# Kernel tuning notes

Measured on AMD Instinct MI355X. Metric: run time of the kernel, lower is better.

Reference implementation:

```python
import jax, jax.numpy as jnp
import numpy as np

N = 1024          # n noisy tokens (seq = 2*N)
DIM = 768
HEADS = 12
HD = DIM // HEADS
BLOCK = 16        # diffusion block size
COND = 128
DFF = 4 * DIM
NEG = -1e30


def rotate_half(x):
    x1, x2 = jnp.split(x, 2, axis=-1)
    return jnp.concatenate((-x2, x1), axis=-1)


def layernorm(x):
    mu = jnp.mean(x, axis=-1, keepdims=True)
    var = jnp.var(x, axis=-1, keepdims=True)
    return (x - mu) * jax.lax.rsqrt(var + 1e-5)


def block_diff_mask(seq, n, block_size):
    idx = jnp.arange(seq)
    q_idx, kv_idx = idx[:, None], idx[None, :]
    fq = q_idx >= n
    fk = kv_idx >= n
    bq = jnp.where(fq, (q_idx - n) // block_size, q_idx // block_size)
    bk = jnp.where(fk, (kv_idx - n) // block_size, kv_idx // block_size)
    block_diagonal = (bq == bk) & (fq == fk)
    offset_block_causal = (bq > bk) & fk & (~fq)
    block_causal = (bq >= bk) & fk & fq
    return block_diagonal | offset_block_causal | block_causal  # [seq, seq] bool


def setup_inputs() -> dict:
    key = jax.random.key(0)
    ks = jax.random.split(key, 12)
    x = jax.random.normal(ks[0], (2, 2 * N, DIM), dtype=jnp.float32)
    c = jax.random.normal(ks[1], (2, COND), dtype=jnp.float32)
    # rotary tables over positions 0..N-1 (each half of the sequence reuses them)
    inv_freq = 1.0 / (10000.0 ** (jnp.arange(0, HD, 2, dtype=jnp.float32) / HD))
    freqs = jnp.arange(N, dtype=jnp.float32)[:, None] * inv_freq[None, :]  # [N, HD/2]
    emb = jnp.concatenate((freqs, freqs), axis=-1)  # [N, HD]
    cos, sin = jnp.cos(emb), jnp.sin(emb)
    s = 0.02
    W_qkv = jax.random.normal(ks[2], (DIM, 3 * DIM), dtype=jnp.float32) * s
    W_out = jax.random.normal(ks[3], (DIM, DIM), dtype=jnp.float32) * s
    ln1_w = jnp.ones((DIM,), dtype=jnp.float32)
    ln2_w = jnp.ones((DIM,), dtype=jnp.float32)
    mlp_w1 = jax.random.normal(ks[4], (DIM, DFF), dtype=jnp.float32) * s
    mlp_b1 = jnp.zeros((DFF,), dtype=jnp.float32)
    mlp_w2 = jax.random.normal(ks[5], (DFF, DIM), dtype=jnp.float32) * s
    mlp_b2 = jnp.zeros((DIM,), dtype=jnp.float32)
    ada_w = jax.random.normal(ks[6], (COND, 6 * DIM), dtype=jnp.float32) * s
    ada_b = jax.random.normal(ks[7], (6 * DIM,), dtype=jnp.float32) * s
    return {"x": x, "cos": cos, "sin": sin, "c": c, "W_qkv": W_qkv, "W_out": W_out,
            "ln1_w": ln1_w, "ln2_w": ln2_w, "mlp_w1": mlp_w1, "mlp_b1": mlp_b1,
            "mlp_w2": mlp_w2, "mlp_b2": mlp_b2, "ada_w": ada_w, "ada_b": ada_b}


def reference(x, cos, sin, c, W_qkv, W_out, ln1_w, ln2_w,
              mlp_w1, mlp_b1, mlp_w2, mlp_b2, ada_w, ada_b):
    b, seq, dim = x.shape
    n = seq // 2
    # adaLN modulation: [b, 1, dim] each (inference: dropout = identity)
    ada = (c @ ada_w + ada_b)[:, None, :]
    shift_msa, scale_msa, gate_msa, shift_mlp, scale_mlp, gate_mlp = jnp.split(ada, 6, axis=2)
    x_skip = x
    h = layernorm(x) * ln1_w
    h = h * (1.0 + scale_msa) + shift_msa  # modulate_fused

    def qkv_rope(seg):
        qkv = (seg @ W_qkv).reshape(b, n, 3, HEADS, HD)
        cs = cos[None, :, None, None, :]
        sn = sin[None, :, None, None, :]
        return qkv * cs + rotate_half(qkv) * sn

    # noisy half and clean (x0) half each get positions 0..n-1
    qkv = jnp.concatenate((qkv_rope(h[:, :n]), qkv_rope(h[:, n:])), axis=1)  # [b,2n,3,H,HD]
    q, k, v = qkv[:, :, 0], qkv[:, :, 1], qkv[:, :, 2]  # [b, 2n, H, HD]
    mask = block_diff_mask(seq, n, BLOCK)  # [2n, 2n]
    scores = jnp.einsum('bqhd,bkhd->bhqk', q, k) / jnp.sqrt(jnp.float32(HD))
    scores = jnp.where(mask[None, None], scores, NEG)
    attn = jax.nn.softmax(scores, axis=-1)
    o = jnp.einsum('bhqk,bkhd->bqhd', attn, v).reshape(b, seq, dim)
    # bias_dropout_add_scale (inference): gate * out + residual
    x1 = gate_msa * (o @ W_out) + x_skip
    h2 = layernorm(x1) * ln2_w
    h2 = h2 * (1.0 + scale_mlp) + shift_mlp
    mlp = jax.nn.gelu(h2 @ mlp_w1 + mlp_b1, approximate=True) @ mlp_w2 + mlp_b2
    return gate_mlp * mlp + x1
```

## Files before the change

### kernel.cpp

```cpp
#include <hip/hip_runtime.h>
#include <hip/hip_bf16.h>
#include <stdint.h>

#define DIM 768
#define SEQ 2048
#define TOKENS 4096
#define HEADS 12
#define DFF 3072
#define COND 128
#define ADA6 4608

typedef __attribute__((ext_vector_type(8))) short bf16x8;
typedef __attribute__((ext_vector_type(4))) float f32x4;

#define MFMA16x32(a, b, c) __builtin_amdgcn_mfma_f32_16x16x32_bf16(a, b, c, 0, 0, 0)
#define GLDS16(g, l)                                                                  \
    __builtin_amdgcn_global_load_lds((const __attribute__((address_space(1))) void*)(g), \
                                     (__attribute__((address_space(3))) void*)(l), 16, 0, 0)

__device__ __forceinline__ ushort f2bf(float f) {
    union { float f; uint32_t u; } v;
    v.f = f;
    uint32_t r = v.u + 0x7FFF + ((v.u >> 16) & 1);
    return (ushort)(r >> 16);
}

__device__ __forceinline__ uint32_t packbf2(float a, float b) {
    union { __hip_bfloat162 h; uint32_t u; } cv;
    cv.h = __float22bfloat162_rn(make_float2(a, b));
    return cv.u;
}

__global__ void ada_kernel(const float* __restrict__ c, const float* __restrict__ ada_w,
                           const float* __restrict__ ada_b, float* __restrict__ ada) {
    int j = blockIdx.x * 256 + threadIdx.x;
    int bb = blockIdx.y;
    if (j < ADA6) {
        float acc = ada_b[j];
        for (int k = 0; k < COND; ++k)
            acc = fmaf(c[bb * COND + k], ada_w[(long)k * ADA6 + j], acc);
        ada[bb * ADA6 + j] = acc;
    }
}

__global__ __launch_bounds__(256) void convT(const float* __restrict__ W,
                                             ushort* __restrict__ Wt, int K, int N) {
    __shared__ float t[64][65];
    int tid = threadIdx.x;
    int n0 = blockIdx.x * 64, k0 = blockIdx.y * 64;
#pragma unroll
    for (int it = 0; it < 4; ++it) {
        int idx = it * 256 + tid;
        int kr = idx >> 4, nc = (idx & 15) * 4;
        float4 v = *(const float4*)&W[(long)(k0 + kr) * N + n0 + nc];
        t[kr][nc] = v.x; t[kr][nc + 1] = v.y; t[kr][nc + 2] = v.z; t[kr][nc + 3] = v.w;
    }
    __syncthreads();
#pragma unroll
    for (int it = 0; it < 4; ++it) {
        int idx = it * 256 + tid;
        int nr = idx >> 4, kc = (idx & 15) * 4;
        ushort4 v;
        v.x = f2bf(t[kc][nr]); v.y = f2bf(t[kc + 1][nr]);
        v.z = f2bf(t[kc + 2][nr]); v.w = f2bf(t[kc + 3][nr]);
        *(ushort4*)&Wt[(long)(n0 + nr) * K + k0 + kc] = v;
    }
}

__global__ __launch_bounds__(256) void ln_mod_kernel(const float* __restrict__ x,
                                                     const float* __restrict__ w,
                                                     const float* __restrict__ ada,
                                                     int shiftOff, int scaleOff,
                                                     ushort* __restrict__ out) {
    int token = blockIdx.x;
    int bb = token >> 11;
    int tid = threadIdx.x;
    const float* xi = x + (long)token * DIM;
    float v[3];
    float sum = 0.f, sumsq = 0.f;
#pragma unroll
    for (int t = 0; t < 3; ++t) {
        float val = xi[tid + 256 * t];
        v[t] = val;
        sum += val;
        sumsq = fmaf(val, val, sumsq);
    }
    for (int msk = 1; msk < 64; msk <<= 1) {
        sum += __shfl_xor(sum, msk, 64);
        sumsq += __shfl_xor(sumsq, msk, 64);
    }
    __shared__ float red0[4], red1[4];
    int wave = tid >> 6;
    if ((tid & 63) == 0) { red0[wave] = sum; red1[wave] = sumsq; }
    __syncthreads();
    sum = red0[0] + red0[1] + red0[2] + red0[3];
    sumsq = red1[0] + red1[1] + red1[2] + red1[3];
    float mu = sum * (1.f / DIM);
    float var = sumsq * (1.f / DIM) - mu * mu;
    float rs = rsqrtf(var + 1e-5f);
    const float* sh = ada + bb * ADA6 + shiftOff;
    const float* sc = ada + bb * ADA6 + scaleOff;
    ushort* oi = out + (long)token * DIM;
#pragma unroll
    for (int t = 0; t < 3; ++t) {
        int j = tid + 256 * t;
        oi[j] = f2bf((v[t] - mu) * rs * w[j] * (1.f + sc[j]) + sh[j]);
    }
}

template <int EPI, int BM>
__global__ __launch_bounds__(256) void gemm_bf16(const ushort* __restrict__ A,
                                                 const ushort* __restrict__ B,
                                                 void* __restrict__ Cp, int M, int N, int K,
                                                 const float* __restrict__ bias,
                                                 const float* __restrict__ gate,
                                                 const float* __restrict__ skip,
                                                 const float* __restrict__ cosT,
                                                 const float* __restrict__ sinT) {
    constexpr int MR = BM / 32;
    __shared__ ushort As[BM * 64];
    __shared__ ushort Bs[128 * 64];
    const int tid = threadIdx.x;
    const int wave = tid >> 6, lane = tid & 63;
    const int lo = lane & 15, hi = lane >> 4;
    const int wr = wave >> 1, wc = wave & 1;
    const int row0 = blockIdx.y * BM, col0 = blockIdx.x * 128;
    const int srow = tid >> 3;
    const int scol = (tid & 7) * 8;
    f32x4 acc[MR][4] = {};
    const long astep = (long)32 * K;
    const ushort* Ag = A + (long)(row0 + srow) * K + scol;
    const ushort* Bg = B + (long)(col0 + srow) * K + scol;
    for (int k0 = 0; k0 < K; k0 += 64) {
        __syncthreads();
#pragma unroll
        for (int t = 0; t < MR; ++t)
            GLDS16(Ag + t * astep + k0, (char*)As + (t * 256 + tid) * 16);
#pragma unroll
        for (int t = 0; t < 4; ++t)
            GLDS16(Bg + t * astep + k0, (char*)Bs + (t * 256 + tid) * 16);
        __syncthreads();
#pragma unroll
        for (int kk = 0; kk < 2; ++kk) {
            bf16x8 af[MR], bfr[4];
#pragma unroll
            for (int m = 0; m < MR; ++m)
                af[m] = *(const bf16x8*)&As[(wr * (BM / 2) + m * 16 + lo) * 64 + kk * 32 + hi * 8];
#pragma unroll
            for (int n = 0; n < 4; ++n)
                bfr[n] = *(const bf16x8*)&Bs[(wc * 64 + n * 16 + lo) * 64 + kk * 32 + hi * 8];
#pragma unroll
            for (int m = 0; m < MR; ++m)
#pragma unroll
                for (int n = 0; n < 4; ++n)
                    acc[m][n] = MFMA16x32(af[m], bfr[n], acc[m][n]);
        }
    }
    if (EPI == 0) {
        ushort* C = (ushort*)Cp;
#pragma unroll
        for (int m = 0; m < MR; ++m)
#pragma unroll
            for (int reg = 0; reg < 4; ++reg) {
                int r = row0 + wr * (BM / 2) + m * 16 + hi * 4 + reg;
                int pos = r & 1023;
                const float* cb = cosT + pos * 64;
                const float* sb = sinT + pos * 64;
                long rb = (long)r * N + col0 + wc * 64;
#pragma unroll
                for (int pr = 0; pr < 2; ++pr) {
                    int i = pr * 16 + lo;
                    float v0 = acc[m][pr][reg], v1 = acc[m][pr + 2][reg];
                    float c0 = cb[i], s0 = sb[i], c1 = cb[i + 32], s1 = sb[i + 32];
                    C[rb + i] = f2bf(v0 * c0 - v1 * s0);
                    C[rb + i + 32] = f2bf(v1 * c1 + v0 * s1);
                }
            }
    } else if (EPI == 1) {
        float* C = (float*)Cp;
#pragma unroll
        for (int m = 0; m < MR; ++m)
#pragma unroll
            for (int reg = 0; reg < 4; ++reg) {
                int r = row0 + wr * (BM / 2) + m * 16 + hi * 4 + reg;
                int bbi = r >> 11;
#pragma unroll
                for (int n = 0; n < 4; ++n) {
                    int c = col0 + wc * 64 + n * 16 + lo;
                    C[(long)r * N + c] =
                        gate[bbi * ADA6 + c] * acc[m][n][reg] + skip[(long)r * DIM + c];
                }
            }
    } else if (EPI == 2) {
        ushort* C = (ushort*)Cp;
#pragma unroll
        for (int m = 0; m < MR; ++m)
#pragma unroll
            for (int reg = 0; reg < 4; ++reg) {
                int r = row0 + wr * (BM / 2) + m * 16 + hi * 4 + reg;
#pragma unroll
                for (int n = 0; n < 4; ++n) {
                    int c = col0 + wc * 64 + n * 16 + lo;
                    float v = acc[m][n][reg] + bias[c];
                    float g = v / (1.f + __expf(-1.5957691216f * (v + 0.044715f * v * v * v)));
                    C[(long)r * N + c] = f2bf(g);
                }
            }
    } else {
        float* C = (float*)Cp;
#pragma unroll
        for (int m = 0; m < MR; ++m)
#pragma unroll
            for (int reg = 0; reg < 4; ++reg) {
                int r = row0 + wr * (BM / 2) + m * 16 + hi * 4 + reg;
                int bbi = r >> 11;
#pragma unroll
                for (int n = 0; n < 4; ++n) {
                    int c = col0 + wc * 64 + n * 16 + lo;
                    C[(long)r * N + c] = gate[bbi * ADA6 + c] * (acc[m][n][reg] + bias[c]) +
                                         skip[(long)r * DIM + c];
                }
            }
    }
}

__global__ __launch_bounds__(256) void vtrans(const ushort* __restrict__ qkv,
                                              ushort* __restrict__ vt) {
    __shared__ ushort t[64][65];
    int tid = threadIdx.x;
    int tb = blockIdx.x;
    int head = blockIdx.y;
    int bb = blockIdx.z;
#pragma unroll
    for (int it = 0; it < 4; ++it) {
        int idx = it * 256 + tid;
        int tok = idx >> 4, d4 = (idx & 15) * 4;
        const ushort* p = qkv + ((long)bb * SEQ + tb * 64 + tok) * 2304 + 1536 + head * 64 + d4;
        ushort4 v = *(const ushort4*)p;
        t[tok][d4] = v.x; t[tok][d4 + 1] = v.y; t[tok][d4 + 2] = v.z; t[tok][d4 + 3] = v.w;
    }
    __syncthreads();
#pragma unroll
    for (int it = 0; it < 4; ++it) {
        int idx = it * 256 + tid;
        int d = idx >> 4, t4 = (idx & 15) * 4;
        ushort4 v;
        v.x = t[t4][d]; v.y = t[t4 + 1][d]; v.z = t[t4 + 2][d]; v.w = t[t4 + 3][d];
        *(ushort4*)&vt[((long)(bb * HEADS + head) * 64 + d) * SEQ + tb * 64 + t4] = v;
    }
}

__global__ __launch_bounds__(256) void attn_mfma(const ushort* __restrict__ qkv,
                                                 const ushort* __restrict__ vt,
                                                 ushort* __restrict__ o) {
    __shared__ char ps[4 * 2048];
    __shared__ float lds_m[4][16], lds_l[4][16];
    __shared__ float lds_o[4][64][16];
    const int tid = threadIdx.x;
    const int wave = tid >> 6, lane = tid & 63;
    const int lo = lane & 15, hi = lane >> 4;
    const int bx = blockIdx.x;
    const int qb = (bx & 1) ? (63 - (bx >> 1)) : (127 - (bx >> 1));
    const int head = blockIdx.y;
    const int bb = blockIdx.z;
    char* psb = ps + wave * 2048;
    const int swz = (lo & 7) << 4;
    const long row0 = (long)bb * SEQ + qb * 16;
    const ushort* Qp = qkv + (row0 + lo) * 2304 + head * 64 + hi * 8;
    bf16x8 qf0 = *(const bf16x8*)Qp;
    bf16x8 qf1 = *(const bf16x8*)(Qp + 32);
    f32x4 oacc[4] = {};
    float m_run = -3.0e38f, l_run = 0.f;
    const ushort* Vbase = vt + (long)(bb * HEADS + head) * 64 * SEQ;

    auto chunk = [&](int base, int valid) {
        const long kr0 = (long)bb * SEQ + base;
        f32x4 s[4] = {};
#pragma unroll
        for (int n = 0; n < 4; ++n) {
            if (n * 16 < valid) {
                const ushort* Kp = qkv + (kr0 + n * 16 + lo) * 2304 + DIM + head * 64 + hi * 8;
                bf16x8 kf0 = *(const bf16x8*)Kp;
                bf16x8 kf1 = *(const bf16x8*)(Kp + 32);
                f32x4 z = {};
                z = MFMA16x32(kf0, qf0, z);
                z = MFMA16x32(kf1, qf1, z);
                s[n] = z;
            }
        }
        float p[4][4];
        float mx = -3.0e38f;
#pragma unroll
        for (int n = 0; n < 4; ++n)
#pragma unroll
            for (int g = 0; g < 4; ++g) {
                float v = (n * 16 < valid) ? s[n][g] * 0.125f : -3.0e38f;
                p[n][g] = v;
                mx = fmaxf(mx, v);
            }
        mx = fmaxf(mx, __shfl_xor(mx, 16, 64));
        mx = fmaxf(mx, __shfl_xor(mx, 32, 64));
        float m_new = fmaxf(m_run, mx);
        float scale = __expf(m_run - m_new);
        float psum = 0.f;
#pragma unroll
        for (int n = 0; n < 4; ++n)
#pragma unroll
            for (int g = 0; g < 4; ++g) {
                float e = __expf(p[n][g] - m_new);
                p[n][g] = e;
                psum += e;
            }
        psum += __shfl_xor(psum, 16, 64);
        psum += __shfl_xor(psum, 32, 64);
        l_run = l_run * scale + psum;
        m_run = m_new;
#pragma unroll
        for (int dt = 0; dt < 4; ++dt) oacc[dt] *= scale;
#pragma unroll
        for (int n = 0; n < 4; ++n)
#pragma unroll
            for (int pr = 0; pr < 2; ++pr) {
                uint32_t u = packbf2(p[n][pr * 2], p[n][pr * 2 + 1]);
                *(uint32_t*)(psb + lo * 128 + ((n * 32 + hi * 8 + pr * 4) ^ swz)) = u;
            }
        bf16x8 pa0 = *(const bf16x8*)(psb + lo * 128 + ((hi * 16) ^ swz));
        bf16x8 pa1 = *(const bf16x8*)(psb + lo * 128 + ((64 + hi * 16) ^ swz));
#pragma unroll
        for (int dt = 0; dt < 4; ++dt) {
            const ushort* Vp = Vbase + (long)(dt * 16 + lo) * SEQ + base + hi * 8;
            bf16x8 v0 = *(const bf16x8*)Vp;
            oacc[dt] = MFMA16x32(v0, pa0, oacc[dt]);
            if (valid > 32) {
                bf16x8 v1 = *(const bf16x8*)(Vp + 32);
                oacc[dt] = MFMA16x32(v1, pa1, oacc[dt]);
            }
        }
    };

    const int R = (qb < 64) ? qb * 16 : (qb - 63) * 16;
    const int Rc = (R + 63) >> 6;
    for (int c = wave; c < Rc; c += 4) chunk(1024 + c * 64, min(64, R - c * 64));
    if (qb < 64 && wave == 3) chunk(qb * 16, 16);

#pragma unroll
    for (int dt = 0; dt < 4; ++dt)
#pragma unroll
        for (int g = 0; g < 4; ++g) lds_o[wave][dt * 16 + hi * 4 + g][lo] = oacc[dt][g];
    if (hi == 0) { lds_m[wave][lo] = m_run; lds_l[wave][lo] = l_run; }
    __syncthreads();
    float m0 = lds_m[0][lo], m1 = lds_m[1][lo], m2 = lds_m[2][lo], m3 = lds_m[3][lo];
    float mt = fmaxf(fmaxf(m0, m1), fmaxf(m2, m3));
    float f0 = __expf(m0 - mt), f1 = __expf(m1 - mt), f2 = __expf(m2 - mt), f3 = __expf(m3 - mt);
    float lt = lds_l[0][lo] * f0 + lds_l[1][lo] * f1 + lds_l[2][lo] * f2 + lds_l[3][lo] * f3;
    float inv = 1.f / lt;
    ushort4 st;
    float a0, a1c, a2, a3;
    {
        int d = wave * 16 + hi * 4;
        a0 = lds_o[0][d][lo] * f0 + lds_o[1][d][lo] * f1 + lds_o[2][d][lo] * f2 + lds_o[3][d][lo] * f3;
        a1c = lds_o[0][d + 1][lo] * f0 + lds_o[1][d + 1][lo] * f1 + lds_o[2][d + 1][lo] * f2 + lds_o[3][d + 1][lo] * f3;
        a2 = lds_o[0][d + 2][lo] * f0 + lds_o[1][d + 2][lo] * f1 + lds_o[2][d + 2][lo] * f2 + lds_o[3][d + 2][lo] * f3;
        a3 = lds_o[0][d + 3][lo] * f0 + lds_o[1][d + 3][lo] * f1 + lds_o[2][d + 3][lo] * f2 + lds_o[3][d + 3][lo] * f3;
    }
    st.x = f2bf(a0 * inv);
    st.y = f2bf(a1c * inv);
    st.z = f2bf(a2 * inv);
    st.w = f2bf(a3 * inv);
    *(ushort4*)&o[(row0 + lo) * DIM + head * 64 + wave * 16 + hi * 4] = st;
}

extern "C" void kernel_launch(void* const* d_in, const int* in_sizes, int n_in,
                              void* d_out, int out_size, void* d_ws, size_t ws_size,
                              hipStream_t stream) {
    const float* x      = (const float*)d_in[0];
    const float* cosT   = (const float*)d_in[1];
    const float* sinT   = (const float*)d_in[2];
    const float* c      = (const float*)d_in[3];
    const float* W_qkv  = (const float*)d_in[4];
    const float* W_out  = (const float*)d_in[5];
    const float* ln1_w  = (const float*)d_in[6];
    const float* ln2_w  = (const float*)d_in[7];
    const float* mlp_w1 = (const float*)d_in[8];
    const float* mlp_b1 = (const float*)d_in[9];
    const float* mlp_w2 = (const float*)d_in[10];
    const float* mlp_b2 = (const float*)d_in[11];
    const float* ada_w  = (const float*)d_in[12];
    const float* ada_b  = (const float*)d_in[13];
    float* out = (float*)d_out;

    char* ws = (char*)d_ws;
    float*  ada   = (float*)(ws + 0);
    ushort* h     = (ushort*)(ws + 65536L);
    ushort* qkv   = (ushort*)(ws + 6356992L);
    ushort* vt    = (ushort*)(ws + 25231360L);
    ushort* o     = (ushort*)(ws + 31522816L);
    float*  x1    = (float*)(ws + 37814272L);
    ushort* a1    = (ushort*)(ws + 50397184L);
    ushort* wqkvT = (ushort*)(ws + 75563008L);
    ushort* woutT = (ushort*)(ws + 79101952L);
    ushort* w1T   = (ushort*)(ws + 80281600L);
    ushort* w2T   = (ushort*)(ws + 85000192L);

    ada_kernel<<<dim3(18, 2), 256, 0, stream>>>(c, ada_w, ada_b, ada);
    convT<<<dim3(36, 12), 256, 0, stream>>>(W_qkv, wqkvT, 768, 2304);
    convT<<<dim3(12, 12), 256, 0, stream>>>(W_out, woutT, 768, 768);
    convT<<<dim3(48, 12), 256, 0, stream>>>(mlp_w1, w1T, 768, 3072);
    convT<<<dim3(12, 48), 256, 0, stream>>>(mlp_w2, w2T, 3072, 768);

    ln_mod_kernel<<<TOKENS, 256, 0, stream>>>(x, ln1_w, ada, 0, 768, h);
    gemm_bf16<0, 128><<<dim3(18, 32), 256, 0, stream>>>(h, wqkvT, qkv, TOKENS, 2304, 768,
                                                        nullptr, nullptr, nullptr, cosT, sinT);
    vtrans<<<dim3(32, 12, 2), 256, 0, stream>>>(qkv, vt);
    attn_mfma<<<dim3(128, 12, 2), 256, 0, stream>>>(qkv, vt, o);
    gemm_bf16<1, 64><<<dim3(6, 64), 256, 0, stream>>>(o, woutT, x1, TOKENS, 768, 768,
                                                      nullptr, ada + 1536, x, nullptr, nullptr);
    ln_mod_kernel<<<TOKENS, 256, 0, stream>>>(x1, ln2_w, ada, 2304, 3072, h);
    gemm_bf16<2, 128><<<dim3(24, 32), 256, 0, stream>>>(h, w1T, a1, TOKENS, DFF, 768,
                                                        mlp_b1, nullptr, nullptr, nullptr, nullptr);
    gemm_bf16<3, 64><<<dim3(6, 64), 256, 0, stream>>>(a1, w2T, out, TOKENS, 768, DFF,
                                                      mlp_b2, ada + 3840, x1, nullptr, nullptr);
}
```

Baseline: 354.8 us.

## Prefetch next K chunk in attention and swizzle GEMM workgroup order

The attention kernel's per-chunk lambda becomes an explicit loop that loads the next chunk's K fragments and the current V fragments ahead of the MFMAs, so global-load latency overlaps compute. Masking moves to per-element validity, and all K/V rows are loaded unconditionally. Separately, the GEMM remaps the flat workgroup id with a stride-8 swizzle to change tile traversal order, likely for L2 or XCD locality. The prefetch adds register pressure and extra loads for partially valid chunks.

Result: no change. 360.7 us (+1.7%).

```diff
diff --git a/kernel.cpp b/kernel.cpp
--- a/kernel.cpp
+++ b/kernel.cpp
@@ -124,7 +124,11 @@
     const int wave = tid >> 6, lane = tid & 63;
     const int lo = lane & 15, hi = lane >> 4;
     const int wr = wave >> 1, wc = wave & 1;
-    const int row0 = blockIdx.y * BM, col0 = blockIdx.x * 128;
+    const int gx = gridDim.x;
+    const int nwg = gx * gridDim.y;
+    const int flat = blockIdx.y * gx + blockIdx.x;
+    const int swzid = (flat & 7) * (nwg >> 3) + (flat >> 3);
+    const int row0 = (swzid / gx) * BM, col0 = (swzid % gx) * 128;
     const int srow = tid >> 3;
     const int scol = (tid & 7) * 8;
     f32x4 acc[MR][4] = {};
@@ -271,22 +275,54 @@
     bf16x8 qf1 = *(const bf16x8*)(Qp + 32);
     f32x4 oacc[4] = {};
     float m_run = -3.0e38f, l_run = 0.f;
-    const ushort* Vbase = vt + (long)(bb * HEADS + head) * 64 * SEQ;
-
-    auto chunk = [&](int base, int valid) {
-        const long kr0 = (long)bb * SEQ + base;
-        f32x4 s[4] = {};
+    const ushort* Kb = qkv + ((long)bb * SEQ + lo) * 2304 + DIM + head * 64 + hi * 8;
+    const ushort* Vbs = vt + ((long)(bb * HEADS + head) * 64 + lo) * SEQ + hi * 8;
+
+    const int R = (qb < 64) ? qb * 16 : (qb - 63) * 16;
+    const int Rc = (R + 63) >> 6;
+    const int nrun = (Rc > wave) ? ((Rc - wave + 3) >> 2) : 0;
+    const bool hdiag = (qb < 64) && (wave == 3);
+    const int nc = nrun + (hdiag ? 1 : 0);
+
+#define CBASE(i) (((i) < nrun) ? (1024 + (wave + 4 * (i)) * 64) : (qb * 16))
+#define CVALID(i) (((i) < nrun) ? (R - (wave + 4 * (i)) * 64) : 16)
+
+    bf16x8 kc[4][2], kn[4][2];
+    if (nc > 0) {
+        const int b0 = CBASE(0);
 #pragma unroll
         for (int n = 0; n < 4; ++n) {
-            if (n * 16 < valid) {
-                const ushort* Kp = qkv + (kr0 + n * 16 + lo) * 2304 + DIM + head * 64 + hi * 8;
-                bf16x8 kf0 = *(const bf16x8*)Kp;
-                bf16x8 kf1 = *(const bf16x8*)(Kp + 32);
-                f32x4 z = {};
-                z = MFMA16x32(kf0, qf0, z);
-                z = MFMA16x32(kf1, qf1, z);
-                s[n] = z;
-            }
+            const ushort* Kp = Kb + (long)(b0 + n * 16) * 2304;
+            kc[n][0] = *(const bf16x8*)Kp;
+            kc[n][1] = *(const bf16x8*)(Kp + 32);
+        }
+    }
+    for (int i = 0; i < nc; ++i) {
+        const int base = CBASE(i);
+        const int valid = min(64, CVALID(i));
+        bf16x8 vf[4][2];
+#pragma unroll
+        for (int dt = 0; dt < 4; ++dt) {
+            const ushort* Vp = Vbs + (long)(dt * 16) * SEQ + base;
+            vf[dt][0] = *(const bf16x8*)Vp;
+            vf[dt][1] = *(const bf16x8*)(Vp + 32);
+        }
+        if (i + 1 < nc) {
+            const int bn = CBASE(i + 1);
+#pragma unroll
+            for (int n = 0; n < 4; ++n) {
+                const ushort* Kp = Kb + (long)(bn + n * 16) * 2304;
+                kn[n][0] = *(const bf16x8*)Kp;
+                kn[n][1] = *(const bf16x8*)(Kp + 32);
+            }
+        }
+        f32x4 s[4];
+#pragma unroll
+        for (int n = 0; n < 4; ++n) {
+            f32x4 z = {};
+            z = MFMA16x32(kc[n][0], qf0, z);
+            z = MFMA16x32(kc[n][1], qf1, z);
+            s[n] = z;
         }
         float p[4][4];
         float mx = -3.0e38f;
@@ -294,7 +330,7 @@
         for (int n = 0; n < 4; ++n)
 #pragma unroll
             for (int g = 0; g < 4; ++g) {
-                float v = (n * 16 < valid) ? s[n][g] * 0.125f : -3.0e38f;
+                float v = (n * 16 + hi * 4 + g < valid) ? s[n][g] * 0.125f : -3.0e38f;
                 p[n][g] = v;
                 mx = fmaxf(mx, v);
             }
@@ -328,20 +364,14 @@
         bf16x8 pa1 = *(const bf16x8*)(psb + lo * 128 + ((64 + hi * 16) ^ swz));
 #pragma unroll
         for (int dt = 0; dt < 4; ++dt) {
-            const ushort* Vp = Vbase + (long)(dt * 16 + lo) * SEQ + base + hi * 8;
-            bf16x8 v0 = *(const bf16x8*)Vp;
-            oacc[dt] = MFMA16x32(v0, pa0, oacc[dt]);
-            if (valid > 32) {
-                bf16x8 v1 = *(const bf16x8*)(Vp + 32);
-                oacc[dt] = MFMA16x32(v1, pa1, oacc[dt]);
-            }
-        }
-    };
-
-    const int R = (qb < 64) ? qb * 16 : (qb - 63) * 16;
-    const int Rc = (R + 63) >> 6;
-    for (int c = wave; c < Rc; c += 4) chunk(1024 + c * 64, min(64, R - c * 64));
-    if (qb < 64 && wave == 3) chunk(qb * 16, 16);
+            oacc[dt] = MFMA16x32(vf[dt][0], pa0, oacc[dt]);
+            oacc[dt] = MFMA16x32(vf[dt][1], pa1, oacc[dt]);
+        }
+#pragma unroll
+        for (int n = 0; n < 4; ++n) { kc[n][0] = kn[n][0]; kc[n][1] = kn[n][1]; }
+    }
+#undef CBASE
+#undef CVALID
 
 #pragma unroll
     for (int dt = 0; dt < 4; ++dt)
```

## Widen attention KV chunks to 128 keys and prefetch K/V before softmax

Applied to the files above, without the earlier changes.

The attention kernel now processes 128-key chunks per wave instead of 64. It issues all K and V fragment loads up front so they overlap the QK MFMAs and the softmax. Partial chunks are masked per element rather than per 16-key tile, and the diagonal 16-key block is handled by a specialised code path that zero-pads the P tile. The per-wave P staging buffer in LDS is doubled and launch bounds request 3 blocks per CU. The extra register pressure from the larger fragment arrays may reduce occupancy or cause spills.

Measured after the change: 353.5 us. No clear change (-0.4%).

```diff
diff --git a/kernel.cpp b/kernel.cpp
--- a/kernel.cpp
+++ b/kernel.cpp
@@ -250,10 +250,10 @@
     }
 }
 
-__global__ __launch_bounds__(256) void attn_mfma(const ushort* __restrict__ qkv,
-                                                 const ushort* __restrict__ vt,
-                                                 ushort* __restrict__ o) {
-    __shared__ char ps[4 * 2048];
+__global__ __launch_bounds__(256, 3) void attn_mfma(const ushort* __restrict__ qkv,
+                                                    const ushort* __restrict__ vt,
+                                                    ushort* __restrict__ o) {
+    __shared__ char ps[4 * 4096];
     __shared__ float lds_m[4][16], lds_l[4][16];
     __shared__ float lds_o[4][64][16];
     const int tid = threadIdx.x;
@@ -263,7 +263,7 @@
     const int qb = (bx & 1) ? (63 - (bx >> 1)) : (127 - (bx >> 1));
     const int head = blockIdx.y;
     const int bb = blockIdx.z;
-    char* psb = ps + wave * 2048;
+    char* psb = ps + wave * 4096;
     const int swz = (lo & 7) << 4;
     const long row0 = (long)bb * SEQ + qb * 16;
     const ushort* Qp = qkv + (row0 + lo) * 2304 + head * 64 + hi * 8;
@@ -271,30 +271,43 @@
     bf16x8 qf1 = *(const bf16x8*)(Qp + 32);
     f32x4 oacc[4] = {};
     float m_run = -3.0e38f, l_run = 0.f;
-    const ushort* Vbase = vt + (long)(bb * HEADS + head) * 64 * SEQ;
-
-    auto chunk = [&](int base, int valid) {
-        const long kr0 = (long)bb * SEQ + base;
-        f32x4 s[4] = {};
-#pragma unroll
-        for (int n = 0; n < 4; ++n) {
-            if (n * 16 < valid) {
-                const ushort* Kp = qkv + (kr0 + n * 16 + lo) * 2304 + DIM + head * 64 + hi * 8;
-                bf16x8 kf0 = *(const bf16x8*)Kp;
-                bf16x8 kf1 = *(const bf16x8*)(Kp + 32);
-                f32x4 z = {};
-                z = MFMA16x32(kf0, qf0, z);
-                z = MFMA16x32(kf1, qf1, z);
-                s[n] = z;
-            }
-        }
-        float p[4][4];
+    const ushort* Kb = qkv + ((long)bb * SEQ + lo) * 2304 + DIM + head * 64 + hi * 8;
+    const ushort* Vbs = vt + ((long)(bb * HEADS + head) * 64 + lo) * SEQ + hi * 8;
+
+    const int R = (qb < 64) ? qb * 16 : (qb - 63) * 16;
+    const int Rc = (R + 127) >> 7;
+
+    for (int c = wave; c < Rc; c += 4) {
+        const int base = 1024 + c * 128;
+        const int valid = min(128, R - c * 128);
+        bf16x8 kf[8][2];
+#pragma unroll
+        for (int n = 0; n < 8; ++n) {
+            const ushort* Kp = Kb + (long)(base + n * 16) * 2304;
+            kf[n][0] = *(const bf16x8*)Kp;
+            kf[n][1] = *(const bf16x8*)(Kp + 32);
+        }
+        f32x4 s[8];
+#pragma unroll
+        for (int n = 0; n < 8; ++n) {
+            f32x4 z = {};
+            z = MFMA16x32(kf[n][0], qf0, z);
+            z = MFMA16x32(kf[n][1], qf1, z);
+            s[n] = z;
+        }
+        bf16x8 vf[4][4];
+#pragma unroll
+        for (int dt = 0; dt < 4; ++dt)
+#pragma unroll
+            for (int g = 0; g < 4; ++g)
+                vf[dt][g] = *(const bf16x8*)(Vbs + (long)(dt * 16) * SEQ + base + g * 32);
+        float p[8][4];
         float mx = -3.0e38f;
 #pragma unroll
-        for (int n = 0; n < 4; ++n)
+        for (int n = 0; n < 8; ++n)
 #pragma unroll
             for (int g = 0; g < 4; ++g) {
-                float v = (n * 16 < valid) ? s[n][g] * 0.125f : -3.0e38f;
+                float v = (n * 16 + hi * 4 + g < valid) ? s[n][g] * 0.125f : -3.0e38f;
                 p[n][g] = v;
                 mx = fmaxf(mx, v);
             }
@@ -304,7 +317,7 @@
         float scale = __expf(m_run - m_new);
         float psum = 0.f;
 #pragma unroll
-        for (int n = 0; n < 4; ++n)
+        for (int n = 0; n < 8; ++n)
 #pragma unroll
             for (int g = 0; g < 4; ++g) {
                 float e = __expf(p[n][g] - m_new);
@@ -318,30 +331,69 @@
 #pragma unroll
         for (int dt = 0; dt < 4; ++dt) oacc[dt] *= scale;
 #pragma unroll
-        for (int n = 0; n < 4; ++n)
+        for (int n = 0; n < 8; ++n)
 #pragma unroll
             for (int pr = 0; pr < 2; ++pr) {
                 uint32_t u = packbf2(p[n][pr * 2], p[n][pr * 2 + 1]);
-                *(uint32_t*)(psb + lo * 128 + ((n * 32 + hi * 8 + pr * 4) ^ swz)) = u;
-            }
-        bf16x8 pa0 = *(const bf16x8*)(psb + lo * 128 + ((hi * 16) ^ swz));
-        bf16x8 pa1 = *(const bf16x8*)(psb + lo * 128 + ((64 + hi * 16) ^ swz));
-#pragma unroll
-        for (int dt = 0; dt < 4; ++dt) {
-            const ushort* Vp = Vbase + (long)(dt * 16 + lo) * SEQ + base + hi * 8;
-            bf16x8 v0 = *(const bf16x8*)Vp;
-            oacc[dt] = MFMA16x32(v0, pa0, oacc[dt]);
-            if (valid > 32) {
-                bf16x8 v1 = *(const bf16x8*)(Vp + 32);
-                oacc[dt] = MFMA16x32(v1, pa1, oacc[dt]);
-            }
-        }
-    };
-
-    const int R = (qb < 64) ? qb * 16 : (qb - 63) * 16;
-    const int Rc = (R + 63) >> 6;
-    for (int c = wave; c < Rc; c += 4) chunk(1024 + c * 64, min(64, R - c * 64));
-    if (qb < 64 && wave == 3) chunk(qb * 16, 16);
+                *(uint32_t*)(psb + lo * 256 + ((n * 32 + hi * 8 + pr * 4) ^ swz)) = u;
+            }
+        bf16x8 pa[4];
+#pragma unroll
+        for (int g = 0; g < 4; ++g)
+            pa[g] = *(const bf16x8*)(psb + lo * 256 + ((g * 64 + hi * 16) ^ swz));
+#pragma unroll
+        for (int dt = 0; dt < 4; ++dt)
+#pragma unroll
+            for (int g = 0; g < 4; ++g)
+                oacc[dt] = MFMA16x32(vf[dt][g], pa[g], oacc[dt]);
+    }
+
+    if (qb < 64 && wave == 3) {
+        const int base = qb * 16;
+        const ushort* Kp = Kb + (long)base * 2304;
+        bf16x8 kf0 = *(const bf16x8*)Kp;
+        bf16x8 kf1 = *(const bf16x8*)(Kp + 32);
+        f32x4 z = {};
+        z = MFMA16x32(kf0, qf0, z);
+        z = MFMA16x32(kf1, qf1, z);
+        bf16x8 vd[4];
+#pragma unroll
+        for (int dt = 0; dt < 4; ++dt)
+            vd[dt] = *(const bf16x8*)(Vbs + (long)(dt * 16) * SEQ + base);
+        float p[4];
+        float mx = -3.0e38f;
+#pragma unroll
+        for (int g = 0; g < 4; ++g) {
+            p[g] = z[g] * 0.125f;
+            mx = fmaxf(mx, p[g]);
+        }
+        mx = fmaxf(mx, __shfl_xor(mx, 16, 64));
+        mx = fmaxf(mx, __shfl_xor(mx, 32, 64));
+        float m_new = fmaxf(m_run, mx);
+        float scale = __expf(m_run - m_new);
+        float psum = 0.f;
+#pragma unroll
+        for (int g = 0; g < 4; ++g) {
+            float e = __expf(p[g] - m_new);
+            p[g] = e;
+            psum += e;
+        }
+        psum += __shfl_xor(psum, 16, 64);
+        psum += __shfl_xor(psum, 32, 64);
+        l_run = l_run * scale + psum;
+        m_run = m_new;
+#pragma unroll
+        for (int dt = 0; dt < 4; ++dt) oacc[dt] *= scale;
+#pragma unroll
+        for (int pr = 0; pr < 2; ++pr) {
+            *(uint32_t*)(psb + lo * 256 + ((hi * 8 + pr * 4) ^ swz)) =
+                packbf2(p[pr * 2], p[pr * 2 + 1]);
+            *(uint32_t*)(psb + lo * 256 + ((32 + hi * 8 + pr * 4) ^ swz)) = 0;
+        }
+        bf16x8 pa0 = *(const bf16x8*)(psb + lo * 256 + ((hi * 16) ^ swz));
+#pragma unroll
+        for (int dt = 0; dt < 4; ++dt) oacc[dt] = MFMA16x32(vd[dt], pa0, oacc[dt]);
+    }
 
 #pragma unroll
     for (int dt = 0; dt < 4; ++dt)
```

## Restructure attention to 64-query tiles with double-buffered LDS K/V staging

Applied to the files above, without the earlier changes.

Each attention block now handles 64 query rows, one 16-row group per wave, instead of 16 rows split across waves by key chunk. K and V chunks are staged into LDS with async global_load_lds and double buffering, so all four waves share each load. This drops the cross-wave softmax merge through LDS and cuts the grid from 128 to 32 blocks in x. The cost is per-chunk barriers and fewer blocks, and the causal and diagonal masking logic is rewritten.

Result: faster. 327.5 us (-7.7%).

```diff
diff --git a/kernel.cpp b/kernel.cpp
--- a/kernel.cpp
+++ b/kernel.cpp
@@ -253,121 +253,145 @@
 __global__ __launch_bounds__(256) void attn_mfma(const ushort* __restrict__ qkv,
                                                  const ushort* __restrict__ vt,
                                                  ushort* __restrict__ o) {
-    __shared__ char ps[4 * 2048];
-    __shared__ float lds_m[4][16], lds_l[4][16];
-    __shared__ float lds_o[4][64][16];
+    __shared__ ushort Ks[2][4096];
+    __shared__ ushort Vs[2][4096];
+    __shared__ char ps[4][2048];
     const int tid = threadIdx.x;
     const int wave = tid >> 6, lane = tid & 63;
     const int lo = lane & 15, hi = lane >> 4;
     const int bx = blockIdx.x;
-    const int qb = (bx & 1) ? (63 - (bx >> 1)) : (127 - (bx >> 1));
+    const int tile = (bx & 1) ? (31 - (bx >> 1)) : (15 - (bx >> 1));
     const int head = blockIdx.y;
     const int bb = blockIdx.z;
-    char* psb = ps + wave * 2048;
+    char* psb = ps[wave];
     const int swz = (lo & 7) << 4;
-    const long row0 = (long)bb * SEQ + qb * 16;
+    const bool fh = tile < 16;
+    const int ncausal = fh ? ((tile * 64 + 111) >> 6) : (tile - 15);
+    const int nchunks = ncausal + (fh ? 1 : 0);
+    const int q0 = tile * 64 + wave * 16;
+    const int vcaus = fh ? q0 : (q0 - 1024 + 16);
+    const long row0 = (long)bb * SEQ + q0;
+
     const ushort* Qp = qkv + (row0 + lo) * 2304 + head * 64 + hi * 8;
     bf16x8 qf0 = *(const bf16x8*)Qp;
     bf16x8 qf1 = *(const bf16x8*)(Qp + 32);
     f32x4 oacc[4] = {};
     float m_run = -3.0e38f, l_run = 0.f;
-    const ushort* Vbase = vt + (long)(bb * HEADS + head) * 64 * SEQ;
-
-    auto chunk = [&](int base, int valid) {
-        const long kr0 = (long)bb * SEQ + base;
-        f32x4 s[4] = {};
-#pragma unroll
-        for (int n = 0; n < 4; ++n) {
-            if (n * 16 < valid) {
-                const ushort* Kp = qkv + (kr0 + n * 16 + lo) * 2304 + DIM + head * 64 + hi * 8;
-                bf16x8 kf0 = *(const bf16x8*)Kp;
-                bf16x8 kf1 = *(const bf16x8*)(Kp + 32);
-                f32x4 z = {};
-                z = MFMA16x32(kf0, qf0, z);
-                z = MFMA16x32(kf1, qf1, z);
-                s[n] = z;
-            }
+
+    const int srow = tid >> 3;
+    const int sc8 = tid & 7;
+    const ushort* Kg = qkv + ((long)bb * SEQ) * 2304 + DIM + head * 64;
+    const ushort* Vg = vt + ((long)(bb * HEADS + head) * 64) * SEQ;
+
+    auto STAGE = [&](int buf, int kbase) {
+#pragma unroll
+        for (int it = 0; it < 2; ++it) {
+            int r = it * 32 + srow;
+            int c8 = sc8 ^ (r & 7);
+            GLDS16(Kg + (long)(kbase + r) * 2304 + c8 * 8,
+                   (char*)Ks[buf] + it * 4096 + tid * 16);
         }
-        float p[4][4];
-        float mx = -3.0e38f;
-#pragma unroll
-        for (int n = 0; n < 4; ++n)
-#pragma unroll
-            for (int g = 0; g < 4; ++g) {
-                float v = (n * 16 < valid) ? s[n][g] * 0.125f : -3.0e38f;
-                p[n][g] = v;
-                mx = fmaxf(mx, v);
-            }
-        mx = fmaxf(mx, __shfl_xor(mx, 16, 64));
-        mx = fmaxf(mx, __shfl_xor(mx, 32, 64));
-        float m_new = fmaxf(m_run, mx);
-        float scale = __expf(m_run - m_new);
-        float psum = 0.f;
-#pragma unroll
-        for (int n = 0; n < 4; ++n)
-#pragma unroll
-            for (int g = 0; g < 4; ++g) {
-                float e = __expf(p[n][g] - m_new);
-                p[n][g] = e;
-                psum += e;
-            }
-        psum += __shfl_xor(psum, 16, 64);
-        psum += __shfl_xor(psum, 32, 64);
-        l_run = l_run * scale + psum;
-        m_run = m_new;
-#pragma unroll
-        for (int dt = 0; dt < 4; ++dt) oacc[dt] *= scale;
-#pragma unroll
-        for (int n = 0; n < 4; ++n)
-#pragma unroll
-            for (int pr = 0; pr < 2; ++pr) {
-                uint32_t u = packbf2(p[n][pr * 2], p[n][pr * 2 + 1]);
-                *(uint32_t*)(psb + lo * 128 + ((n * 32 + hi * 8 + pr * 4) ^ swz)) = u;
-            }
-        bf16x8 pa0 = *(const bf16x8*)(psb + lo * 128 + ((hi * 16) ^ swz));
-        bf16x8 pa1 = *(const bf16x8*)(psb + lo * 128 + ((64 + hi * 16) ^ swz));
-#pragma unroll
-        for (int dt = 0; dt < 4; ++dt) {
-            const ushort* Vp = Vbase + (long)(dt * 16 + lo) * SEQ + base + hi * 8;
-            bf16x8 v0 = *(const bf16x8*)Vp;
-            oacc[dt] = MFMA16x32(v0, pa0, oacc[dt]);
-            if (valid > 32) {
-                bf16x8 v1 = *(const bf16x8*)(Vp + 32);
-                oacc[dt] = MFMA16x32(v1, pa1, oacc[dt]);
-            }
+#pragma unroll
+        for (int it = 0; it < 2; ++it) {
+            int r = it * 32 + srow;
+            int c8 = sc8 ^ (r & 7);
+            GLDS16(Vg + (long)r * SEQ + kbase + c8 * 8,
+                   (char*)Vs[buf] + it * 4096 + tid * 16);
         }
     };
-
-    const int R = (qb < 64) ? qb * 16 : (qb - 63) * 16;
-    const int Rc = (R + 63) >> 6;
-    for (int c = wave; c < Rc; c += 4) chunk(1024 + c * 64, min(64, R - c * 64));
-    if (qb < 64 && wave == 3) chunk(qb * 16, 16);
-
-#pragma unroll
-    for (int dt = 0; dt < 4; ++dt)
-#pragma unroll
-        for (int g = 0; g < 4; ++g) lds_o[wave][dt * 16 + hi * 4 + g][lo] = oacc[dt][g];
-    if (hi == 0) { lds_m[wave][lo] = m_run; lds_l[wave][lo] = l_run; }
-    __syncthreads();
-    float m0 = lds_m[0][lo], m1 = lds_m[1][lo], m2 = lds_m[2][lo], m3 = lds_m[3][lo];
-    float mt = fmaxf(fmaxf(m0, m1), fmaxf(m2, m3));
-    float f0 = __expf(m0 - mt), f1 = __expf(m1 - mt), f2 = __expf(m2 - mt), f3 = __expf(m3 - mt);
-    float lt = lds_l[0][lo] * f0 + lds_l[1][lo] * f1 + lds_l[2][lo] * f2 + lds_l[3][lo] * f3;
-    float inv = 1.f / lt;
-    ushort4 st;
-    float a0, a1c, a2, a3;
-    {
-        int d = wave * 16 + hi * 4;
-        a0 = lds_o[0][d][lo] * f0 + lds_o[1][d][lo] * f1 + lds_o[2][d][lo] * f2 + lds_o[3][d][lo] * f3;
-        a1c = lds_o[0][d + 1][lo] * f0 + lds_o[1][d + 1][lo] * f1 + lds_o[2][d + 1][lo] * f2 + lds_o[3][d + 1][lo] * f3;
-        a2 = lds_o[0][d + 2][lo] * f0 + lds_o[1][d + 2][lo] * f1 + lds_o[2][d + 2][lo] * f2 + lds_o[3][d + 2][lo] * f3;
-        a3 = lds_o[0][d + 3][lo] * f0 + lds_o[1][d + 3][lo] * f1 + lds_o[2][d + 3][lo] * f2 + lds_o[3][d + 3][lo] * f3;
-    }
-    st.x = f2bf(a0 * inv);
-    st.y = f2bf(a1c * inv);
-    st.z = f2bf(a2 * inv);
-    st.w = f2bf(a3 * inv);
-    *(ushort4*)&o[(row0 + lo) * DIM + head * 64 + wave * 16 + hi * 4] = st;
+#define KB(cc) (((cc) < ncausal) ? (1024 + (cc) * 64) : (tile * 64))
+
+    STAGE(0, KB(0));
+    for (int c = 0; c < nchunks; ++c) {
+        const int cur = c & 1;
+        if (c + 1 < nchunks) {
+            STAGE(1 - cur, KB(c + 1));
+            asm volatile("s_waitcnt vmcnt(4)" ::: "memory");
+        } else {
+            asm volatile("s_waitcnt vmcnt(0)" ::: "memory");
+        }
+        __builtin_amdgcn_s_barrier();
+        __builtin_amdgcn_sched_barrier(0);
+        const bool isdiag = (c >= ncausal);
+        const int v = isdiag ? 16 : (vcaus - c * 64);
+        if (v > 0) {
+            f32x4 s4[4];
+#pragma unroll
+            for (int n = 0; n < 4; ++n) {
+                f32x4 z = {};
+#pragma unroll
+                for (int kk = 0; kk < 2; ++kk) {
+                    const bf16x8 kf = *(const bf16x8*)((const char*)Ks[cur] +
+                        ((n * 16 + lo) << 7) + ((((kk << 2) + hi) ^ (lo & 7)) << 4));
+                    z = MFMA16x32(kf, kk ? qf1 : qf0, z);
+                }
+                s4[n] = z;
+            }
+            const int vv = isdiag ? 64 : min(v, 64);
+            float p[4][4];
+            float mx = -3.0e38f;
+#pragma unroll
+            for (int n = 0; n < 4; ++n)
+#pragma unroll
+                for (int g = 0; g < 4; ++g) {
+                    bool ok = isdiag ? (n == wave) : (n * 16 + hi * 4 + g < vv);
+                    float val = ok ? s4[n][g] * 0.125f : -3.0e38f;
+                    p[n][g] = val;
+                    mx = fmaxf(mx, val);
+                }
+            mx = fmaxf(mx, __shfl_xor(mx, 16, 64));
+            mx = fmaxf(mx, __shfl_xor(mx, 32, 64));
+            float m_new = fmaxf(m_run, mx);
+            float scale = __expf(m_run - m_new);
+            float psum = 0.f;
+#pragma unroll
+            for (int n = 0; n < 4; ++n)
+#pragma unroll
+                for (int g = 0; g < 4; ++g) {
+                    float e = __expf(p[n][g] - m_new);
+                    p[n][g] = e;
+                    psum += e;
+                }
+            psum += __shfl_xor(psum, 16, 64);
+            psum += __shfl_xor(psum, 32, 64);
+            l_run = l_run * scale + psum;
+            m_run = m_new;
+#pragma unroll
+            for (int dt = 0; dt < 4; ++dt) oacc[dt] *= scale;
+#pragma unroll
+            for (int n = 0; n < 4; ++n)
+#pragma unroll
+                for (int pr = 0; pr < 2; ++pr) {
+                    uint32_t u = packbf2(p[n][pr * 2], p[n][pr * 2 + 1]);
+                    *(uint32_t*)(psb + lo * 128 + ((n * 32 + hi * 8 + pr * 4) ^ swz)) = u;
+                }
+            bf16x8 pa0 = *(const bf16x8*)(psb + lo * 128 + ((hi * 16) ^ swz));
+            bf16x8 pa1 = *(const bf16x8*)(psb + lo * 128 + ((64 + hi * 16) ^ swz));
+#pragma unroll
+            for (int dt = 0; dt < 4; ++dt) {
+#pragma unroll
+                for (int kk = 0; kk < 2; ++kk) {
+                    const bf16x8 vf = *(const bf16x8*)((const char*)Vs[cur] +
+                        ((dt * 16 + lo) << 7) + ((((kk << 2) + hi) ^ (lo & 7)) << 4));
+                    oacc[dt] = MFMA16x32(vf, kk ? pa1 : pa0, oacc[dt]);
+                }
+            }
+        }
+        __builtin_amdgcn_s_barrier();
+        __builtin_amdgcn_sched_barrier(0);
+    }
+#undef KB
+
+    float inv = 1.f / l_run;
+#pragma unroll
+    for (int dt = 0; dt < 4; ++dt) {
+        ushort4 st;
+        st.x = f2bf(oacc[dt][0] * inv);
+        st.y = f2bf(oacc[dt][1] * inv);
+        st.z = f2bf(oacc[dt][2] * inv);
+        st.w = f2bf(oacc[dt][3] * inv);
+        *(ushort4*)&o[(row0 + lo) * DIM + head * 64 + dt * 16 + hi * 4] = st;
+    }
 }
 
 extern "C" void kernel_launch(void* const* d_in, const int* in_sizes, int n_in,
@@ -412,7 +436,7 @@
     gemm_bf16<0, 128><<<dim3(18, 32), 256, 0, stream>>>(h, wqkvT, qkv, TOKENS, 2304, 768,
                                                         nullptr, nullptr, nullptr, cosT, sinT);
     vtrans<<<dim3(32, 12, 2), 256, 0, stream>>>(qkv, vt);
-    attn_mfma<<<dim3(128, 12, 2), 256, 0, stream>>>(qkv, vt, o);
+    attn_mfma<<<dim3(32, 12, 2), 256, 0, stream>>>(qkv, vt, o);
     gemm_bf16<1, 64><<<dim3(6, 64), 256, 0, stream>>>(o, woutT, x1, TOKENS, 768, 768,
                                                       nullptr, ada + 1536, x, nullptr, nullptr);
     ln_mod_kernel<<<TOKENS, 256, 0, stream>>>(x1, ln2_w, ada, 2304, 3072, h);
```
